# Optimization experiments

Hardware: AMD Instinct MI355X
Metric: run time of the kernel (lower is better)

## Reference

```python
import jax, jax.numpy as jnp
import numpy as np

RES = [64, 128, 256, 512, 1024]   # per-level grid resolutions
NF = 8                            # n_features per level
NC = 2                            # n_cells (staggered grid copies)
P = 1_000_000                     # number of query points


def setup_inputs() -> dict:
    key = jax.random.key(0)
    ks = jax.random.split(key, 2 + len(RES))
    x = jax.random.uniform(ks[0], (P, 1), dtype=jnp.float32)
    y = jax.random.uniform(ks[1], (P, 1), dtype=jnp.float32)
    inp = {"x": x, "y": y}
    for i, r in enumerate(RES):
        # F_active[i]: uniform in [-1e-5, 1e-5], shape (n_cells, n_features, r, r)
        inp[f"table{i}"] = jax.random.uniform(
            ks[2 + i], (NC, NF, r, r), dtype=jnp.float32, minval=-1e-5, maxval=1e-5)
    return inp


def _sample_level(table, xn, yn):
    """Manual bilinear grid_sample (align_corners=True) with per-cell staggered
    sub-pixel offsets (offset=True in the original grid_sample_2d).
    table: (nc, C, H, W); xn, yn: (P,) in [-1, 1]. Returns (P, C)."""
    nc, C, H, W = table.shape
    off = jnp.arange(nc, dtype=xn.dtype) / nc              # staggered offsets in pixels
    ix = (xn + 1.0) * 0.5 * (W - 1) + off[:, None]         # (nc, P) pixel coords
    iy = (yn + 1.0) * 0.5 * (H - 1) + off[:, None]
    x0 = jnp.floor(ix)
    y0 = jnp.floor(iy)
    wx = ix - x0                                            # bilinear weights (nc, P)
    wy = iy - y0
    x0i = jnp.clip(x0.astype(jnp.int32), 0, W - 1)
    x1i = jnp.clip(x0i + 1, 0, W - 1)
    y0i = jnp.clip(y0.astype(jnp.int32), 0, H - 1)
    y1i = jnp.clip(y0i + 1, 0, H - 1)

    def per_cell(tab, x0i, x1i, y0i, y1i, wx, wy):
        t = tab.reshape(C, H * W)                           # (C, HW)
        g = lambda yi, xi: t[:, yi * W + xi]                # gather -> (C, P)
        nw = g(y0i, x0i); ne = g(y0i, x1i)
        sw = g(y1i, x0i); se = g(y1i, x1i)
        return (nw * (1 - wx) * (1 - wy) + ne * wx * (1 - wy)
                + sw * (1 - wx) * wy + se * wx * wy)        # (C, P)

    feats = jax.vmap(per_cell)(table, x0i, x1i, y0i, y1i, wx, wy)  # (nc, C, P)
    return feats.sum(0).T                                   # sum over cells -> (P, C)


def reference(x, y, table0, table1, table2, table3, table4):
    # domain_size = [0,1,0,1] -> normalize to [-1, 1]
    xn = (x * 2.0 - 1.0)[:, 0]
    yn = (y * 2.0 - 1.0)[:, 0]
    tables = [table0, table1, table2, table3, table4]
    # concat per-level features along feature dim -> (P, NF * len(RES))
    return jnp.concatenate([_sample_level(t, xn, yn) for t in tables], axis=1)
```

## Files before the change

### kernel.cpp

```cpp
#include <hip/hip_runtime.h>


#define WS_CURS 0
#define WS_OVFC 16384
#define WS_DEQ 16448
#define WS_INV 16480
#define WS_PART 20480
#define WS_OVF 65536
#define WS_SLOT 589824
#define WS_TAB 15532032
#define WS_END_BF16 60227584ull
#define WS_END_I8 37879808ull
#define NGRP 4096
#define CAP 304
#define OVF_CAP 131072
#define LDS_CAP 1600
#define NSCAT_BF16 4096
#define NSCAT_I8 2048

typedef __attribute__((ext_vector_type(8))) unsigned short ushort8v;

__device__ __forceinline__ unsigned short f2bf(float f) {
  union { float f; unsigned u; } c; c.f = f;
  unsigned u = c.u;
  u += 0x7FFFu + ((u >> 16) & 1u);
  return (unsigned short)(u >> 16);
}

__device__ __forceinline__ void scatter_one(
    const float* __restrict__ x, const float* __restrict__ y, int p,
    unsigned* __restrict__ cursor, unsigned* __restrict__ ovf_cnt,
    int* __restrict__ ovf, float* __restrict__ slots) {
  float xv = x[p], yv = y[p];
  int bx = min(max((int)(xv * 128.0f), 0), 127);
  int by = min(max((int)(yv * 128.0f), 0), 127);
  int g = (by >> 1) * 64 + (bx >> 1);
  unsigned s = atomicAdd(&cursor[g], 1u);
  if (s < CAP) {
    float* sp = slots + ((size_t)g * CAP + s) * 3u;
    sp[0] = xv * 2.0f - 1.0f;
    sp[1] = yv * 2.0f - 1.0f;
    sp[2] = __int_as_float(p);
  } else {
    unsigned o = atomicAdd(ovf_cnt, 1u);
    if (o < OVF_CAP) ovf[o] = p;
  }
}

__global__ __launch_bounds__(256) void transform_scatter_kernel(
    const float* __restrict__ s0, const float* __restrict__ s1,
    const float* __restrict__ s2, const float* __restrict__ s3,
    const float* __restrict__ s4, uint4* __restrict__ tb,
    const float* __restrict__ x, const float* __restrict__ y, int P,
    unsigned* __restrict__ cursor, unsigned* __restrict__ ovf_cnt,
    int* __restrict__ ovf, float* __restrict__ slots) {
  int b = blockIdx.x;
  if (b < NSCAT_BF16) {
    int stride = NSCAT_BF16 * 256;
    for (int p = b * 256 + (int)threadIdx.x; p < P; p += stride)
      scatter_one(x, y, p, cursor, ovf_cnt, ovf, slots);
    return;
  }
  int bb = b - NSCAT_BF16;
  const float* src; int HW; int lb; size_t toff;
  if (bb < 32)        { src = s0; HW = 4096;    lb = 0;    toff = 0; }
  else if (bb < 160)  { src = s1; HW = 16384;   lb = 32;   toff = 8192; }
  else if (bb < 672)  { src = s2; HW = 65536;   lb = 160;  toff = 40960; }
  else if (bb < 2720) { src = s3; HW = 262144;  lb = 672;  toff = 172032; }
  else                { src = s4; HW = 1048576; lb = 2720; toff = 696320; }
  int i = (bb - lb) * 256 + (int)threadIdx.x;
  int cell = i / HW;
  int pix = i - cell * HW;
  const float* s = src + (size_t)cell * 8u * (size_t)HW + (size_t)pix;
  ushort8v v;
#pragma unroll
  for (int ch = 0; ch < 8; ++ch) v[ch] = f2bf(s[(size_t)ch * HW]);
  ((ushort8v*)tb)[toff + (size_t)i] = v;
}

struct Win { int ixmin, iymin, ww, wh, base; };

template <int W>
__device__ __forceinline__ Win mkwin(float xlo, float xhi, float ylo, float yhi,
                                     int base) {
  const float s = (float)(W - 1);
  Win w;
  w.ixmin = max(0, (int)floorf(xlo * s) - 1);
  int ixmax = min(W - 1, (int)floorf(xhi * s + 0.5f) + 2);
  w.iymin = max(0, (int)floorf(ylo * s) - 1);
  int iymax = min(W - 1, (int)floorf(yhi * s + 0.5f) + 2);
  w.ww = ixmax - w.ixmin + 1;
  w.wh = iymax - w.iymin + 1;
  w.base = base;
  return w;
}

__device__ __forceinline__ void store8(float* __restrict__ o,
                                       const float* __restrict__ r) {
  ((float4*)o)[0] = make_float4(r[0], r[1], r[2], r[3]);
  ((float4*)o)[1] = make_float4(r[4], r[5], r[6], r[7]);
}

template <int W>
__device__ __forceinline__ void stage_bf16(uint4* __restrict__ lds, const Win& w,
                                           const uint4* __restrict__ t) {
  int n = w.ww * w.wh;
  for (int j = (int)threadIdx.x; j < 2 * n; j += 256) {
    int cell = j >= n;
    int jj = cell ? j - n : j;
    int r = jj / w.ww;
    int c = jj - r * w.ww;
    lds[w.base + j] = t[cell * W * W + (w.iymin + r) * W + (w.ixmin + c)];
  }
}

__device__ __forceinline__ void fma_bf(uint4 v, float w, float* __restrict__ acc) {
  acc[0] = fmaf(__uint_as_float(v.x << 16), w, acc[0]);
  acc[1] = fmaf(__uint_as_float(v.x & 0xFFFF0000u), w, acc[1]);
  acc[2] = fmaf(__uint_as_float(v.y << 16), w, acc[2]);
  acc[3] = fmaf(__uint_as_float(v.y & 0xFFFF0000u), w, acc[3]);
  acc[4] = fmaf(__uint_as_float(v.z << 16), w, acc[4]);
  acc[5] = fmaf(__uint_as_float(v.z & 0xFFFF0000u), w, acc[5]);
  acc[6] = fmaf(__uint_as_float(v.w << 16), w, acc[6]);
  acc[7] = fmaf(__uint_as_float(v.w & 0xFFFF0000u), w, acc[7]);
}

template <int W>
__device__ __forceinline__ void sample_bf_lds(const uint4* __restrict__ lds,
                                              const Win& w, float xn, float yn,
                                              float* __restrict__ res) {
  const float s = (float)(W - 1);
  float acc[8];
#pragma unroll
  for (int i = 0; i < 8; ++i) acc[i] = 0.0f;
#pragma unroll
  for (int cell = 0; cell < 2; ++cell) {
    const float off = 0.5f * (float)cell;
    float ix = (xn + 1.0f) * 0.5f * s + off;
    float iy = (yn + 1.0f) * 0.5f * s + off;
    float xf = floorf(ix), yf = floorf(iy);
    float wx = ix - xf, wy = iy - yf;
    int x0 = min(max((int)xf, 0), W - 1);
    int y0 = min(max((int)yf, 0), W - 1);
    int x1 = min(x0 + 1, W - 1);
    int y1 = min(y0 + 1, W - 1);
    int cb = w.base + cell * (w.ww * w.wh) - w.ixmin;
    int r0 = cb + (y0 - w.iymin) * w.ww;
    int r1 = cb + (y1 - w.iymin) * w.ww;
    uint4 c00 = lds[r0 + x0], c01 = lds[r0 + x1];
    uint4 c10 = lds[r1 + x0], c11 = lds[r1 + x1];
    float w00 = (1.0f - wx) * (1.0f - wy);
    float w01 = wx * (1.0f - wy);
    float w10 = (1.0f - wx) * wy;
    float w11 = wx * wy;
    fma_bf(c00, w00, acc);
    fma_bf(c01, w01, acc);
    fma_bf(c10, w10, acc);
    fma_bf(c11, w11, acc);
  }
#pragma unroll
  for (int i = 0; i < 8; ++i) res[i] = acc[i];
}

template <int W>
__device__ __forceinline__ void sample_bf_glob(const uint4* __restrict__ t,
                                               float xn, float yn,
                                               float* __restrict__ res) {
  const float s = (float)(W - 1);
  float acc[8];
#pragma unroll
  for (int i = 0; i < 8; ++i) acc[i] = 0.0f;
#pragma unroll
  for (int cell = 0; cell < 2; ++cell) {
    const float off = 0.5f * (float)cell;
    float ix = (xn + 1.0f) * 0.5f * s + off;
    float iy = (yn + 1.0f) * 0.5f * s + off;
    float xf = floorf(ix), yf = floorf(iy);
    float wx = ix - xf, wy = iy - yf;
    int x0 = min(max((int)xf, 0), W - 1);
    int y0 = min(max((int)yf, 0), W - 1);
    int x1 = min(x0 + 1, W - 1);
    int y1 = min(y0 + 1, W - 1);
    const uint4* b = t + cell * W * W;
    uint4 c00 = b[y0 * W + x0], c01 = b[y0 * W + x1];
    uint4 c10 = b[y1 * W + x0], c11 = b[y1 * W + x1];
    float w00 = (1.0f - wx) * (1.0f - wy);
    float w01 = wx * (1.0f - wy);
    float w10 = (1.0f - wx) * wy;
    float w11 = wx * wy;
    fma_bf(c00, w00, acc);
    fma_bf(c01, w01, acc);
    fma_bf(c10, w10, acc);
    fma_bf(c11, w11, acc);
  }
#pragma unroll
  for (int i = 0; i < 8; ++i) res[i] = acc[i];
}

__global__ __launch_bounds__(256) void sample_tile_bf16(
    const float* __restrict__ slots, const unsigned* __restrict__ cursor,
    const unsigned* __restrict__ ovf_cnt, const int* __restrict__ ovf,
    const float* __restrict__ x, const float* __restrict__ y,
    const uint4* __restrict__ t0, const uint4* __restrict__ t1,
    const uint4* __restrict__ t2, const uint4* __restrict__ t3,
    const uint4* __restrict__ t4, float* __restrict__ out, int P) {
  __shared__ uint4 lds[LDS_CAP];
  int g = blockIdx.x;

  if (g >= NGRP) {
    int n = min((int)*ovf_cnt, OVF_CAP);
    int stride = (gridDim.x - NGRP) * 256;
    for (int i = (g - NGRP) * 256 + (int)threadIdx.x; i < n; i += stride) {
      int p = ovf[i];
      float xn = x[p] * 2.0f - 1.0f;
      float yn = y[p] * 2.0f - 1.0f;
      float* orow = out + (size_t)p * 40u;
      float res[8];
      sample_bf_glob<64>(t0, xn, yn, res);   store8(orow + 0, res);
      sample_bf_glob<128>(t1, xn, yn, res);  store8(orow + 8, res);
      sample_bf_glob<256>(t2, xn, yn, res);  store8(orow + 16, res);
      sample_bf_glob<512>(t3, xn, yn, res);  store8(orow + 24, res);
      sample_bf_glob<1024>(t4, xn, yn, res); store8(orow + 32, res);
    }
    return;
  }

  int cnt = min((int)cursor[g], CAP);
  if (cnt == 0) return;

  int gx = g & 63, gy = g >> 6;
  float xlo = (float)gx * (1.0f / 64.0f);
  float xhi = (float)(gx + 1) * (1.0f / 64.0f);
  float ylo = (float)gy * (1.0f / 64.0f);
  float yhi = (float)(gy + 1) * (1.0f / 64.0f);

  Win w0 = mkwin<64>(xlo, xhi, ylo, yhi, 0);
  Win w1 = mkwin<128>(xlo, xhi, ylo, yhi, w0.base + 2 * w0.ww * w0.wh);
  Win w2 = mkwin<256>(xlo, xhi, ylo, yhi, w1.base + 2 * w1.ww * w1.wh);
  Win w3 = mkwin<512>(xlo, xhi, ylo, yhi, w2.base + 2 * w2.ww * w2.wh);
  Win w4 = mkwin<1024>(xlo, xhi, ylo, yhi, w3.base + 2 * w3.ww * w3.wh);
  int total = w4.base + 2 * w4.ww * w4.wh;
  bool use_lds = (total <= LDS_CAP);

  if (use_lds) {
    stage_bf16<64>(lds, w0, t0);
    stage_bf16<128>(lds, w1, t1);
    stage_bf16<256>(lds, w2, t2);
    stage_bf16<512>(lds, w3, t3);
    stage_bf16<1024>(lds, w4, t4);
    __syncthreads();
  }

  const float* gs = slots + (size_t)g * CAP * 3u;
  for (int i = (int)threadIdx.x; i < cnt; i += 256) {
    const float* sp = gs + (size_t)i * 3u;
    float xn = sp[0], yn = sp[1];
    int q = __float_as_int(sp[2]);
    float* orow = out + (size_t)q * 40u;
    float res[8];
    if (use_lds) {
      sample_bf_lds<64>(lds, w0, xn, yn, res);   store8(orow + 0, res);
      sample_bf_lds<128>(lds, w1, xn, yn, res);  store8(orow + 8, res);
      sample_bf_lds<256>(lds, w2, xn, yn, res);  store8(orow + 16, res);
      sample_bf_lds<512>(lds, w3, xn, yn, res);  store8(orow + 24, res);
      sample_bf_lds<1024>(lds, w4, xn, yn, res); store8(orow + 32, res);
    } else {
      sample_bf_glob<64>(t0, xn, yn, res);   store8(orow + 0, res);
      sample_bf_glob<128>(t1, xn, yn, res);  store8(orow + 8, res);
      sample_bf_glob<256>(t2, xn, yn, res);  store8(orow + 16, res);
      sample_bf_glob<512>(t3, xn, yn, res);  store8(orow + 24, res);
      sample_bf_glob<1024>(t4, xn, yn, res); store8(orow + 32, res);
    }
  }
}

__global__ __launch_bounds__(256) void absmax_scatter_kernel(
    const float* __restrict__ s0, const float* __restrict__ s1,
    const float* __restrict__ s2, const float* __restrict__ s3,
    const float* __restrict__ s4, unsigned* __restrict__ partials,
    const float* __restrict__ x, const float* __restrict__ y, int P,
    unsigned* __restrict__ cursor, unsigned* __restrict__ ovf_cnt,
    int* __restrict__ ovf, float* __restrict__ slots) {
  int b = blockIdx.x;
  if (b < NSCAT_I8) {
    int stride = NSCAT_I8 * 256;
    for (int p = b * 256 + (int)threadIdx.x; p < P; p += stride)
      scatter_one(x, y, p, cursor, ovf_cnt, ovf, slots);
    return;
  }
  int bb = b - NSCAT_I8;
  __shared__ unsigned red[4];
  const float* src; int n4; int lb; int nb;
  if (bb < 16)        { src = s0; n4 = 16384;   lb = 0;    nb = 16; }
  else if (bb < 80)   { src = s1; n4 = 65536;   lb = 16;   nb = 64; }
  else if (bb < 336)  { src = s2; n4 = 262144;  lb = 80;   nb = 256; }
  else if (bb < 1360) { src = s3; n4 = 1048576; lb = 336;  nb = 1024; }
  else                { src = s4; n4 = 4194304; lb = 1360; nb = 4096; }
  int local = bb - lb;
  unsigned m = 0;
  for (int k = local * 256 + threadIdx.x; k < n4; k += nb * 256) {
    float4 v = ((const float4*)src)[k];
    unsigned a = __float_as_uint(v.x) & 0x7FFFFFFFu;
    unsigned c = __float_as_uint(v.y) & 0x7FFFFFFFu;
    unsigned d = __float_as_uint(v.z) & 0x7FFFFFFFu;
    unsigned e = __float_as_uint(v.w) & 0x7FFFFFFFu;
    m = max(m, max(max(a, c), max(d, e)));
  }
#pragma unroll
  for (int off = 32; off; off >>= 1)
    m = max(m, (unsigned)__shfl_xor((int)m, off));
  if ((threadIdx.x & 63) == 0) red[threadIdx.x >> 6] = m;
  __syncthreads();
  if (threadIdx.x == 0)
    partials[bb] = max(max(red[0], red[1]), max(red[2], red[3]));
}

__global__ __launch_bounds__(256) void finalize_scales_kernel(
    const unsigned* __restrict__ partials, float* __restrict__ deq,
    float* __restrict__ inv) {
  __shared__ unsigned red[4];
  int t = (int)threadIdx.x;
  const int lo[5] = {0, 16, 80, 336, 1360};
  const int hi[5] = {16, 80, 336, 1360, 5456};
  for (int l = 0; l < 5; ++l) {
    unsigned m = 0;
    for (int i = lo[l] + t; i < hi[l]; i += 256) m = max(m, partials[i]);
#pragma unroll
    for (int off = 32; off; off >>= 1)
      m = max(m, (unsigned)__shfl_xor((int)m, off));
    if ((t & 63) == 0) red[t >> 6] = m;
    __syncthreads();
    if (t == 0) {
      unsigned r = max(max(red[0], red[1]), max(red[2], red[3]));
      float s = __uint_as_float(r);
      if (!(s > 0.0f)) s = 1e-20f;
      deq[l] = s / 127.0f;
      inv[l] = 127.0f / s;
    }
    __syncthreads();
  }
}

__global__ __launch_bounds__(256) void quant_kernel(
    const float* __restrict__ s0, const float* __restrict__ s1,
    const float* __restrict__ s2, const float* __restrict__ s3,
    const float* __restrict__ s4, uint2* __restrict__ tb,
    const float* __restrict__ invp) {
  int b = blockIdx.x;
  const float* src; int HW; int lb; int l; size_t toff;
  if (b < 32)        { src = s0; HW = 4096;    lb = 0;    l = 0; toff = 0; }
  else if (b < 160)  { src = s1; HW = 16384;   lb = 32;   l = 1; toff = 8192; }
  else if (b < 672)  { src = s2; HW = 65536;   lb = 160;  l = 2; toff = 40960; }
  else if (b < 2720) { src = s3; HW = 262144;  lb = 672;  l = 3; toff = 172032; }
  else               { src = s4; HW = 1048576; lb = 2720; l = 4; toff = 696320; }
  int i = (b - lb) * 256 + (int)threadIdx.x;
  float sc = invp[l];
  int cell = i / HW;
  int pix = i - cell * HW;
  const float* s = src + (size_t)cell * 8u * (size_t)HW + (size_t)pix;
  unsigned lov = 0, hiv = 0;
#pragma unroll
  for (int c = 0; c < 4; ++c) {
    int q = (int)rintf(s[(size_t)c * HW] * sc);
    q = min(max(q, -127), 127);
    lov |= ((unsigned)(q & 0xFF)) << (8 * c);
  }
#pragma unroll
  for (int c = 0; c < 4; ++c) {
    int q = (int)rintf(s[(size_t)(c + 4) * HW] * sc);
    q = min(max(q, -127), 127);
    hiv |= ((unsigned)(q & 0xFF)) << (8 * c);
  }
  tb[toff + (size_t)i] = make_uint2(lov, hiv);
}

template <int W>
__device__ __forceinline__ void stage_i8(uint2* __restrict__ lds, const Win& w,
                                         const uint2* __restrict__ t) {
  int n = w.ww * w.wh;
  for (int i = (int)threadIdx.x; i < 2 * n; i += 256) {
    int cell = i >= n;
    int j = cell ? i - n : i;
    int r = j / w.ww;
    int c = j - r * w.ww;
    lds[w.base + i] = t[cell * W * W + (w.iymin + r) * W + (w.ixmin + c)];
  }
}

__device__ __forceinline__ void fma_i8(unsigned lo, unsigned hi, float w,
                                       float* __restrict__ acc) {
#pragma unroll
  for (int c = 0; c < 4; ++c)
    acc[c] = fmaf((float)(signed char)(lo >> (8 * c)), w, acc[c]);
#pragma unroll
  for (int c = 0; c < 4; ++c)
    acc[4 + c] = fmaf((float)(signed char)(hi >> (8 * c)), w, acc[4 + c]);
}

template <int W>
__device__ __forceinline__ void sample_i8(const uint2* __restrict__ lds,
                                          const Win& w, bool use_lds,
                                          const uint2* __restrict__ t,
                                          float xn, float yn, float deq,
                                          float* __restrict__ res) {
  const float s = (float)(W - 1);
  float acc[8];
#pragma unroll
  for (int i = 0; i < 8; ++i) acc[i] = 0.0f;
#pragma unroll
  for (int cell = 0; cell < 2; ++cell) {
    const float off = 0.5f * (float)cell;
    float ix = (xn + 1.0f) * 0.5f * s + off;
    float iy = (yn + 1.0f) * 0.5f * s + off;
    float xf = floorf(ix), yf = floorf(iy);
    float wx = ix - xf, wy = iy - yf;
    int x0 = min(max((int)xf, 0), W - 1);
    int y0 = min(max((int)yf, 0), W - 1);
    int x1 = min(x0 + 1, W - 1);
    int y1 = min(y0 + 1, W - 1);
    uint2 c00, c01, c10, c11;
    if (use_lds) {
      int cb = w.base + cell * (w.ww * w.wh) - w.ixmin;
      int r0 = cb + (y0 - w.iymin) * w.ww;
      int r1 = cb + (y1 - w.iymin) * w.ww;
      c00 = lds[r0 + x0]; c01 = lds[r0 + x1];
      c10 = lds[r1 + x0]; c11 = lds[r1 + x1];
    } else {
      const uint2* b = t + cell * W * W;
      c00 = b[y0 * W + x0]; c01 = b[y0 * W + x1];
      c10 = b[y1 * W + x0]; c11 = b[y1 * W + x1];
    }
    float w00 = (1.0f - wx) * (1.0f - wy);
    float w01 = wx * (1.0f - wy);
    float w10 = (1.0f - wx) * wy;
    float w11 = wx * wy;
    fma_i8(c00.x, c00.y, w00, acc);
    fma_i8(c01.x, c01.y, w01, acc);
    fma_i8(c10.x, c10.y, w10, acc);
    fma_i8(c11.x, c11.y, w11, acc);
  }
#pragma unroll
  for (int i = 0; i < 8; ++i) res[i] = acc[i] * deq;
}

__global__ __launch_bounds__(256) void sample_tile_i8(
    const float* __restrict__ slots, const unsigned* __restrict__ cursor,
    const unsigned* __restrict__ ovf_cnt, const int* __restrict__ ovf,
    const float* __restrict__ x, const float* __restrict__ y,
    const uint2* __restrict__ t0, const uint2* __restrict__ t1,
    const uint2* __restrict__ t2, const uint2* __restrict__ t3,
    const uint2* __restrict__ t4, const float* __restrict__ deqs,
    float* __restrict__ out, int P) {
  __shared__ uint2 lds[LDS_CAP];
  int g = blockIdx.x;
  float d0 = deqs[0], d1 = deqs[1], d2 = deqs[2], d3 = deqs[3], d4 = deqs[4];
  Win wdum = {0, 0, 1, 1, 0};

  if (g >= NGRP) {
    int n = min((int)*ovf_cnt, OVF_CAP);
    int stride = (gridDim.x - NGRP) * 256;
    for (int i = (g - NGRP) * 256 + (int)threadIdx.x; i < n; i += stride) {
      int p = ovf[i];
      float xn = x[p] * 2.0f - 1.0f;
      float yn = y[p] * 2.0f - 1.0f;
      float* orow = out + (size_t)p * 40u;
      float res[8];
      sample_i8<64>(lds, wdum, false, t0, xn, yn, d0, res);   store8(orow + 0, res);
      sample_i8<128>(lds, wdum, false, t1, xn, yn, d1, res);  store8(orow + 8, res);
      sample_i8<256>(lds, wdum, false, t2, xn, yn, d2, res);  store8(orow + 16, res);
      sample_i8<512>(lds, wdum, false, t3, xn, yn, d3, res);  store8(orow + 24, res);
      sample_i8<1024>(lds, wdum, false, t4, xn, yn, d4, res); store8(orow + 32, res);
    }
    return;
  }

  int cnt = min((int)cursor[g], CAP);
  if (cnt == 0) return;

  int gx = g & 63, gy = g >> 6;
  float xlo = (float)gx * (1.0f / 64.0f);
  float xhi = (float)(gx + 1) * (1.0f / 64.0f);
  float ylo = (float)gy * (1.0f / 64.0f);
  float yhi = (float)(gy + 1) * (1.0f / 64.0f);

  Win w0 = mkwin<64>(xlo, xhi, ylo, yhi, 0);
  Win w1 = mkwin<128>(xlo, xhi, ylo, yhi, w0.base + 2 * w0.ww * w0.wh);
  Win w2 = mkwin<256>(xlo, xhi, ylo, yhi, w1.base + 2 * w1.ww * w1.wh);
  Win w3 = mkwin<512>(xlo, xhi, ylo, yhi, w2.base + 2 * w2.ww * w2.wh);
  Win w4 = mkwin<1024>(xlo, xhi, ylo, yhi, w3.base + 2 * w3.ww * w3.wh);
  int total = w4.base + 2 * w4.ww * w4.wh;
  bool use_lds = (total <= LDS_CAP);

  if (use_lds) {
    stage_i8<64>(lds, w0, t0);
    stage_i8<128>(lds, w1, t1);
    stage_i8<256>(lds, w2, t2);
    stage_i8<512>(lds, w3, t3);
    stage_i8<1024>(lds, w4, t4);
    __syncthreads();
  }

  const float* gs = slots + (size_t)g * CAP * 3u;
  for (int i = (int)threadIdx.x; i < cnt; i += 256) {
    const float* sp = gs + (size_t)i * 3u;
    float xn = sp[0], yn = sp[1];
    int q = __float_as_int(sp[2]);
    float* orow = out + (size_t)q * 40u;
    float res[8];
    sample_i8<64>(lds, w0, use_lds, t0, xn, yn, d0, res);   store8(orow + 0, res);
    sample_i8<128>(lds, w1, use_lds, t1, xn, yn, d1, res);  store8(orow + 8, res);
    sample_i8<256>(lds, w2, use_lds, t2, xn, yn, d2, res);  store8(orow + 16, res);
    sample_i8<512>(lds, w3, use_lds, t3, xn, yn, d3, res);  store8(orow + 24, res);
    sample_i8<1024>(lds, w4, use_lds, t4, xn, yn, d4, res); store8(orow + 32, res);
  }
}

template <int W>
__device__ __forceinline__ void sample_level_direct(
    const float* __restrict__ t, float xv, float yv, float* __restrict__ o) {
  float acc[8];
#pragma unroll
  for (int i = 0; i < 8; ++i) acc[i] = 0.0f;
  float xn = xv * 2.0f - 1.0f;
  float yn = yv * 2.0f - 1.0f;
#pragma unroll
  for (int cell = 0; cell < 2; ++cell) {
    const float off = 0.5f * (float)cell;
    float ix = (xn + 1.0f) * 0.5f * (float)(W - 1) + off;
    float iy = (yn + 1.0f) * 0.5f * (float)(W - 1) + off;
    float x0f = floorf(ix), y0f = floorf(iy);
    float wx = ix - x0f, wy = iy - y0f;
    int x0 = (int)x0f; x0 = min(max(x0, 0), W - 1);
    int y0 = (int)y0f; y0 = min(max(y0, 0), W - 1);
    int x1 = min(x0 + 1, W - 1);
    int y1 = min(y0 + 1, W - 1);
    float w00 = (1.0f - wx) * (1.0f - wy);
    float w01 = wx * (1.0f - wy);
    float w10 = (1.0f - wx) * wy;
    float w11 = wx * wy;
    size_t i00 = (size_t)y0 * W + x0;
    size_t i01 = (size_t)y0 * W + x1;
    size_t i10 = (size_t)y1 * W + x0;
    size_t i11 = (size_t)y1 * W + x1;
#pragma unroll
    for (int c = 0; c < 8; ++c) {
      const float* pc = t + (size_t)cell * 8u * (size_t)W * (size_t)W +
                        (size_t)c * (size_t)W * (size_t)W;
      acc[c] += pc[i00] * w00 + pc[i01] * w01 + pc[i10] * w10 + pc[i11] * w11;
    }
  }
#pragma unroll
  for (int i = 0; i < 8; ++i) o[i] = acc[i];
}

__global__ __launch_bounds__(256) void sample_kernel_direct(
    const float* __restrict__ x, const float* __restrict__ y,
    const float* __restrict__ t0, const float* __restrict__ t1,
    const float* __restrict__ t2, const float* __restrict__ t3,
    const float* __restrict__ t4, float* __restrict__ out, int P) {
  int p = blockIdx.x * blockDim.x + threadIdx.x;
  if (p >= P) return;
  float xv = x[p];
  float yv = y[p];
  float o[8];
  float* orow = out + (size_t)p * 40u;
  sample_level_direct<64>(t0, xv, yv, o);
#pragma unroll
  for (int i = 0; i < 8; ++i) orow[0 + i] = o[i];
  sample_level_direct<128>(t1, xv, yv, o);
#pragma unroll
  for (int i = 0; i < 8; ++i) orow[8 + i] = o[i];
  sample_level_direct<256>(t2, xv, yv, o);
#pragma unroll
  for (int i = 0; i < 8; ++i) orow[16 + i] = o[i];
  sample_level_direct<512>(t3, xv, yv, o);
#pragma unroll
  for (int i = 0; i < 8; ++i) orow[24 + i] = o[i];
  sample_level_direct<1024>(t4, xv, yv, o);
#pragma unroll
  for (int i = 0; i < 8; ++i) orow[32 + i] = o[i];
}

extern "C" void kernel_launch(void* const* d_in, const int* in_sizes, int n_in,
                              void* d_out, int out_size, void* d_ws, size_t ws_size,
                              hipStream_t stream) {
  const float* x = (const float*)d_in[0];
  const float* y = (const float*)d_in[1];
  const float* tabs[5] = {(const float*)d_in[2], (const float*)d_in[3],
                          (const float*)d_in[4], (const float*)d_in[5],
                          (const float*)d_in[6]};
  float* out = (float*)d_out;
  const int P = in_sizes[0];

  const size_t offs[5] = {0, 8192, 40960, 172032, 696320};

  unsigned* cursor = (unsigned*)((char*)d_ws + WS_CURS);
  unsigned* ovf_cnt = (unsigned*)((char*)d_ws + WS_OVFC);
  int* ovf = (int*)((char*)d_ws + WS_OVF);
  float* slots = (float*)((char*)d_ws + WS_SLOT);

  if (ws_size >= WS_END_BF16 && P <= 1000448) {
    uint4* tb = (uint4*)((char*)d_ws + WS_TAB);
    (void)hipMemsetAsync((char*)d_ws, 0, WS_OVFC + 4, stream);
    transform_scatter_kernel<<<NSCAT_BF16 + 10912, 256, 0, stream>>>(
        tabs[0], tabs[1], tabs[2], tabs[3], tabs[4], tb, x, y, P, cursor,
        ovf_cnt, ovf, slots);
    sample_tile_bf16<<<NGRP + 32, 256, 0, stream>>>(
        slots, cursor, ovf_cnt, ovf, x, y, tb + offs[0], tb + offs[1],
        tb + offs[2], tb + offs[3], tb + offs[4], out, P);
  } else if (ws_size >= WS_END_I8 && P <= 1000448) {
    float* deq = (float*)((char*)d_ws + WS_DEQ);
    float* inv = (float*)((char*)d_ws + WS_INV);
    unsigned* partials = (unsigned*)((char*)d_ws + WS_PART);
    uint2* tb = (uint2*)((char*)d_ws + WS_TAB);
    (void)hipMemsetAsync((char*)d_ws, 0, WS_OVFC + 4, stream);
    absmax_scatter_kernel<<<NSCAT_I8 + 5456, 256, 0, stream>>>(
        tabs[0], tabs[1], tabs[2], tabs[3], tabs[4], partials, x, y, P, cursor,
        ovf_cnt, ovf, slots);
    finalize_scales_kernel<<<1, 256, 0, stream>>>(partials, deq, inv);
    quant_kernel<<<10912, 256, 0, stream>>>(
        tabs[0], tabs[1], tabs[2], tabs[3], tabs[4], tb, inv);
    sample_tile_i8<<<NGRP + 32, 256, 0, stream>>>(
        slots, cursor, ovf_cnt, ovf, x, y, tb + offs[0], tb + offs[1],
        tb + offs[2], tb + offs[3], tb + offs[4], deq, out, P);
  } else {
    sample_kernel_direct<<<(P + 255) / 256, 256, 0, stream>>>(
        x, y, tabs[0], tabs[1], tabs[2], tabs[3], tabs[4], out, P);
  }
}
```

Baseline: 188.6 us.

## Aggregate scatter binning per block with LDS histograms before global atomics

Point scattering switches from one global atomic per point across 4096 blocks to 64 blocks. Each block builds an LDS histogram over its chunk of points, reserves slot ranges with one global atomic per bin, then writes points using LDS atomics for local ranks. This is meant to cut global atomic contention on the bin cursors. The cost is that only 64 blocks handle about 1M points with two passes over x and y, which may leave the scatter phase underparallelised and on the critical path, and the transform blocks must wait behind these long-running blocks.

```diff
diff --git a/kernel.cpp b/kernel.cpp
--- a/kernel.cpp
+++ b/kernel.cpp
@@ -15,7 +15,7 @@
 #define CAP 304
 #define OVF_CAP 131072
 #define LDS_CAP 1600
-#define NSCAT_BF16 4096
+#define NSCAT 64
 #define NSCAT_I8 2048
 
 typedef __attribute__((ext_vector_type(8))) unsigned short ushort8v;
@@ -27,14 +27,18 @@
   return (unsigned short)(u >> 16);
 }
 
+__device__ __forceinline__ int bin_of(float xv, float yv) {
+  int bx = min(max((int)(xv * 128.0f), 0), 127);
+  int by = min(max((int)(yv * 128.0f), 0), 127);
+  return (by >> 1) * 64 + (bx >> 1);
+}
+
 __device__ __forceinline__ void scatter_one(
     const float* __restrict__ x, const float* __restrict__ y, int p,
     unsigned* __restrict__ cursor, unsigned* __restrict__ ovf_cnt,
     int* __restrict__ ovf, float* __restrict__ slots) {
   float xv = x[p], yv = y[p];
-  int bx = min(max((int)(xv * 128.0f), 0), 127);
-  int by = min(max((int)(yv * 128.0f), 0), 127);
-  int g = (by >> 1) * 64 + (bx >> 1);
+  int g = bin_of(xv, yv);
   unsigned s = atomicAdd(&cursor[g], 1u);
   if (s < CAP) {
     float* sp = slots + ((size_t)g * CAP + s) * 3u;
@@ -54,14 +58,44 @@
     const float* __restrict__ x, const float* __restrict__ y, int P,
     unsigned* __restrict__ cursor, unsigned* __restrict__ ovf_cnt,
     int* __restrict__ ovf, float* __restrict__ slots) {
+  __shared__ unsigned cnt[NGRP];
+  __shared__ unsigned base[NGRP];
   int b = blockIdx.x;
-  if (b < NSCAT_BF16) {
-    int stride = NSCAT_BF16 * 256;
-    for (int p = b * 256 + (int)threadIdx.x; p < P; p += stride)
-      scatter_one(x, y, p, cursor, ovf_cnt, ovf, slots);
+  if (b < NSCAT) {
+    int chunk = (P + NSCAT - 1) / NSCAT;
+    int lo = b * chunk;
+    int hi = min(lo + chunk, P);
+    int tid = (int)threadIdx.x;
+    for (int i = tid; i < NGRP; i += 256) cnt[i] = 0u;
+    __syncthreads();
+    for (int p = lo + tid; p < hi; p += 256)
+      atomicAdd(&cnt[bin_of(x[p], y[p])], 1u);
+    __syncthreads();
+    for (int g = tid; g < NGRP; g += 256) {
+      unsigned c = cnt[g];
+      base[g] = c ? atomicAdd(&cursor[g], c) : 0u;
+    }
+    __syncthreads();
+    for (int i = tid; i < NGRP; i += 256) cnt[i] = 0u;
+    __syncthreads();
+    for (int p = lo + tid; p < hi; p += 256) {
+      float xv = x[p], yv = y[p];
+      int g = bin_of(xv, yv);
+      unsigned r = atomicAdd(&cnt[g], 1u);
+      unsigned idx = base[g] + r;
+      if (idx < CAP) {
+        float* sp = slots + ((size_t)g * CAP + idx) * 3u;
+        sp[0] = xv * 2.0f - 1.0f;
+        sp[1] = yv * 2.0f - 1.0f;
+        sp[2] = __int_as_float(p);
+      } else {
+        unsigned o = atomicAdd(ovf_cnt, 1u);
+        if (o < OVF_CAP) ovf[o] = p;
+      }
+    }
     return;
   }
-  int bb = b - NSCAT_BF16;
+  int bb = b - NSCAT;
   const float* src; int HW; int lb; size_t toff;
   if (bb < 32)        { src = s0; HW = 4096;    lb = 0;    toff = 0; }
   else if (bb < 160)  { src = s1; HW = 16384;   lb = 32;   toff = 8192; }
@@ -602,7 +636,7 @@
   if (ws_size >= WS_END_BF16 && P <= 1000448) {
     uint4* tb = (uint4*)((char*)d_ws + WS_TAB);
     (void)hipMemsetAsync((char*)d_ws, 0, WS_OVFC + 4, stream);
-    transform_scatter_kernel<<<NSCAT_BF16 + 10912, 256, 0, stream>>>(
+    transform_scatter_kernel<<<NSCAT + 10912, 256, 0, stream>>>(
         tabs[0], tabs[1], tabs[2], tabs[3], tabs[4], tb, x, y, P, cursor,
         ovf_cnt, ovf, slots);
     sample_tile_bf16<<<NGRP + 32, 256, 0, stream>>>(
```

Measured after the change: 171.2 us. 1.1x faster.
